# Kernel tuning notes

Measured on AMD Instinct MI355X. Metric: run time of the kernel, lower is better.

## Reference

```python
import jax, jax.numpy as jnp
import numpy as np

B, G, IN, NC, OUT = 32768, 25, 128, 3, 75
# group id per in_out_map entry: 0=spinal (0-4), 1=nfn (5-14), 2=ss (15-24)
GROUP = jnp.asarray(np.repeat(np.arange(3), [5, 10, 10]).astype(np.int32))


def _linear_init(key, fan_in, shape):
    s = 1.0 / np.sqrt(fan_in)
    return jax.random.uniform(key, shape, minval=-s, maxval=s, dtype=jnp.float32)


def setup_inputs() -> dict:
    key = jax.random.key(0)
    ks = jax.random.split(key, 7)
    x = jax.random.normal(ks[0], (B, G * IN), dtype=jnp.float32)
    # in_out_map: entry i gathers contiguous block i of width IN, scatters to slots 3i..3i+2
    K = jnp.arange(G * IN, dtype=jnp.int32).reshape(G, IN)
    V = jnp.arange(G * NC, dtype=jnp.int32).reshape(G, NC)
    W_spinal = _linear_init(ks[1], IN, (IN, NC))
    b_spinal = _linear_init(ks[2], IN, (NC,))
    W_nfn = _linear_init(ks[3], IN, (IN, NC))
    b_nfn = _linear_init(ks[4], IN, (NC,))
    W_ss = _linear_init(ks[5], IN, (IN, NC))
    b_ss = _linear_init(ks[6], IN, (NC,))
    return dict(x=x, K=K, V=V, W_spinal=W_spinal, b_spinal=b_spinal,
                W_nfn=W_nfn, b_nfn=b_nfn, W_ss=W_ss, b_ss=b_ss)


def reference(x, K, V, W_spinal, b_spinal, W_nfn, b_nfn, W_ss, b_ss):
    # Stack the 3 tiny Linears and broadcast to one weight per map entry: (G, IN, NC)
    W = jnp.stack([W_spinal, W_nfn, W_ss])[GROUP]
    b = jnp.stack([b_spinal, b_nfn, b_ss])[GROUP]        # (G, NC)
    xg = x[:, K]                                         # gather -> (B, G, IN)
    o = jnp.einsum('bgi,gic->bgc', xg, W) + b            # (B, G, NC)
    out = jnp.zeros((x.shape[0], OUT), x.dtype)
    out = out.at[:, V.reshape(-1)].set(o.reshape(x.shape[0], G * 3))  # scatter
    return out
```

## Files before the change

kernel.cpp:

```cpp
#include <hip/hip_runtime.h>


#define NSEG      819200
#define NCHUNK    102400
#define GRID_DIM  2048
#define BLOCK_DIM 256

__global__ __launch_bounds__(BLOCK_DIM, 8)
void mlp_rsna9_kernel(const float* __restrict__ x,
                      const float* __restrict__ Wsp, const float* __restrict__ bsp,
                      const float* __restrict__ Wnf, const float* __restrict__ bnf,
                      const float* __restrict__ Wss, const float* __restrict__ bss,
                      float* __restrict__ out)
{
    __shared__ __align__(16) float w_lds[3 * 3 * 128];
    __shared__ float b_lds[12];

    const int tid = threadIdx.x;

    for (int idx = tid; idx < 1152; idx += BLOCK_DIM) {
        int t = idx / 384;
        int r = idx - t * 384;
        int c = r >> 7;
        int i = r & 127;
        const float* wp = (t == 0) ? Wsp : (t == 1) ? Wnf : Wss;
        w_lds[idx] = wp[i * 3 + c];
    }
    if (tid < 9) {
        int t = tid / 3;
        int c = tid - t * 3;
        const float* bp = (t == 0) ? bsp : (t == 1) ? bnf : bss;
        b_lds[tid] = bp[c];
    }
    __syncthreads();

    const int half = tid >> 5;
    const int i0   = (tid & 31) << 2;

    for (int chunk = blockIdx.x; chunk < NCHUNK; chunk += gridDim.x) {
        const int seg = chunk * 8 + half;
        const int g   = seg % 25;
        const int t   = (g >= 5) + (g >= 15);

        const float4 xv = *(const float4*)(x + (size_t)chunk * 1024 + (size_t)tid * 4);

        const float* wb = w_lds + t * 384 + i0;
        const float4 w0 = *(const float4*)(wb);
        const float4 w1 = *(const float4*)(wb + 128);
        const float4 w2 = *(const float4*)(wb + 256);

        float a0 = xv.x * w0.x + xv.y * w0.y + xv.z * w0.z + xv.w * w0.w;
        float a1 = xv.x * w1.x + xv.y * w1.y + xv.z * w1.z + xv.w * w1.w;
        float a2 = xv.x * w2.x + xv.y * w2.y + xv.z * w2.z + xv.w * w2.w;

        #pragma unroll
        for (int m = 16; m >= 1; m >>= 1) {
            a0 += __shfl_xor(a0, m, 64);
            a1 += __shfl_xor(a1, m, 64);
            a2 += __shfl_xor(a2, m, 64);
        }

        if ((tid & 31) == 0) {
            float* op = out + (size_t)seg * 3;
            op[0] = a0 + b_lds[t * 3 + 0];
            op[1] = a1 + b_lds[t * 3 + 1];
            op[2] = a2 + b_lds[t * 3 + 2];
        }
    }
}

extern "C" void kernel_launch(void* const* d_in, const int* in_sizes, int n_in,
                              void* d_out, int out_size, void* d_ws, size_t ws_size,
                              hipStream_t stream)
{
    const float* x   = (const float*)d_in[0];
    const float* Wsp = (const float*)d_in[3];
    const float* bsp = (const float*)d_in[4];
    const float* Wnf = (const float*)d_in[5];
    const float* bnf = (const float*)d_in[6];
    const float* Wss = (const float*)d_in[7];
    const float* bss = (const float*)d_in[8];
    float* out = (float*)d_out;

    mlp_rsna9_kernel<<<GRID_DIM, BLOCK_DIM, 0, stream>>>(
        x, Wsp, bsp, Wnf, bnf, Wss, bss, out);
}
```

Baseline: 564.4 us.

## Process two chunks per iteration and reduce with DPP instead of shuffles

Each block iteration now loads and computes two 1024-float chunks, so each thread has two independent global loads in flight. The cross-lane reduction over each 32-lane half switches from __shfl_xor (LDS permute) to DPP row-shift adds plus a row broadcast, with the result landing in lane 31. This aims to hide memory latency and cut reduction instruction cost, at the price of more registers and reliance on exact DPP lane semantics.

```diff
diff --git a/kernel.cpp b/kernel.cpp
--- a/kernel.cpp
+++ b/kernel.cpp
@@ -1,10 +1,25 @@
 #include <hip/hip_runtime.h>
 
 
-#define NSEG      819200
 #define NCHUNK    102400
 #define GRID_DIM  2048
 #define BLOCK_DIM 256
+
+#define FADD_DPP(acc, ctrl, rmask)                                             \
+  do {                                                                         \
+    int _t = __builtin_amdgcn_update_dpp(0, __float_as_int(acc), (ctrl),       \
+                                         (rmask), 0xF, true);                  \
+    (acc) += __int_as_float(_t);                                               \
+  } while (0)
+
+#define HALF_REDUCE3(a0, a1, a2)                                               \
+  do {                                                                         \
+    FADD_DPP(a0, 0x111, 0xF); FADD_DPP(a1, 0x111, 0xF); FADD_DPP(a2, 0x111, 0xF); \
+    FADD_DPP(a0, 0x112, 0xF); FADD_DPP(a1, 0x112, 0xF); FADD_DPP(a2, 0x112, 0xF); \
+    FADD_DPP(a0, 0x114, 0xF); FADD_DPP(a1, 0x114, 0xF); FADD_DPP(a2, 0x114, 0xF); \
+    FADD_DPP(a0, 0x118, 0xF); FADD_DPP(a1, 0x118, 0xF); FADD_DPP(a2, 0x118, 0xF); \
+    FADD_DPP(a0, 0x142, 0xA); FADD_DPP(a1, 0x142, 0xA); FADD_DPP(a2, 0x142, 0xA); \
+  } while (0)
 
 __global__ __launch_bounds__(BLOCK_DIM, 8)
 void mlp_rsna9_kernel(const float* __restrict__ x,
@@ -37,34 +52,47 @@
     const int half = tid >> 5;
     const int i0   = (tid & 31) << 2;
 
-    for (int chunk = blockIdx.x; chunk < NCHUNK; chunk += gridDim.x) {
-        const int seg = chunk * 8 + half;
-        const int g   = seg % 25;
-        const int t   = (g >= 5) + (g >= 15);
+    for (int base = blockIdx.x * 2; base < NCHUNK; base += GRID_DIM * 2) {
+        const int c0 = base, c1 = base + 1;
 
-        const float4 xv = *(const float4*)(x + (size_t)chunk * 1024 + (size_t)tid * 4);
+        const float4 xv0 = *(const float4*)(x + (size_t)c0 * 1024 + (size_t)tid * 4);
+        const float4 xv1 = *(const float4*)(x + (size_t)c1 * 1024 + (size_t)tid * 4);
 
-        const float* wb = w_lds + t * 384 + i0;
-        const float4 w0 = *(const float4*)(wb);
-        const float4 w1 = *(const float4*)(wb + 128);
-        const float4 w2 = *(const float4*)(wb + 256);
+        const int seg0 = c0 * 8 + half;
+        const int seg1 = c1 * 8 + half;
+        const int g0 = seg0 % 25;
+        const int g1 = seg1 % 25;
+        const int t0 = (g0 >= 5) + (g0 >= 15);
+        const int t1 = (g1 >= 5) + (g1 >= 15);
 
-        float a0 = xv.x * w0.x + xv.y * w0.y + xv.z * w0.z + xv.w * w0.w;
-        float a1 = xv.x * w1.x + xv.y * w1.y + xv.z * w1.z + xv.w * w1.w;
-        float a2 = xv.x * w2.x + xv.y * w2.y + xv.z * w2.z + xv.w * w2.w;
+        const float* wb0 = w_lds + t0 * 384 + i0;
+        const float4 w00 = *(const float4*)(wb0);
+        const float4 w01 = *(const float4*)(wb0 + 128);
+        const float4 w02 = *(const float4*)(wb0 + 256);
+        const float* wb1 = w_lds + t1 * 384 + i0;
+        const float4 w10 = *(const float4*)(wb1);
+        const float4 w11 = *(const float4*)(wb1 + 128);
+        const float4 w12 = *(const float4*)(wb1 + 256);
 
-        #pragma unroll
-        for (int m = 16; m >= 1; m >>= 1) {
-            a0 += __shfl_xor(a0, m, 64);
-            a1 += __shfl_xor(a1, m, 64);
-            a2 += __shfl_xor(a2, m, 64);
-        }
+        float a00 = xv0.x * w00.x + xv0.y * w00.y + xv0.z * w00.z + xv0.w * w00.w;
+        float a01 = xv0.x * w01.x + xv0.y * w01.y + xv0.z * w01.z + xv0.w * w01.w;
+        float a02 = xv0.x * w02.x + xv0.y * w02.y + xv0.z * w02.z + xv0.w * w02.w;
+        float a10 = xv1.x * w10.x + xv1.y * w10.y + xv1.z * w10.z + xv1.w * w10.w;
+        float a11 = xv1.x * w11.x + xv1.y * w11.y + xv1.z * w11.z + xv1.w * w11.w;
+        float a12 = xv1.x * w12.x + xv1.y * w12.y + xv1.z * w12.z + xv1.w * w12.w;
 
-        if ((tid & 31) == 0) {
-            float* op = out + (size_t)seg * 3;
-            op[0] = a0 + b_lds[t * 3 + 0];
-            op[1] = a1 + b_lds[t * 3 + 1];
-            op[2] = a2 + b_lds[t * 3 + 2];
+        HALF_REDUCE3(a00, a01, a02);
+        HALF_REDUCE3(a10, a11, a12);
+
+        if ((tid & 31) == 31) {
+            float* op0 = out + (size_t)seg0 * 3;
+            op0[0] = a00 + b_lds[t0 * 3 + 0];
+            op0[1] = a01 + b_lds[t0 * 3 + 1];
+            op0[2] = a02 + b_lds[t0 * 3 + 2];
+            float* op1 = out + (size_t)seg1 * 3;
+            op1[0] = a10 + b_lds[t1 * 3 + 0];
+            op1[1] = a11 + b_lds[t1 * 3 + 1];
+            op1[2] = a12 + b_lds[t1 * 3 + 2];
         }
     }
 }
```

Result: no change. 560.9 us (-0.6%).
